# Kernel optimization log

Hardware: AMD Instinct MI355X
Metric: run time of the kernel (lower is better)

Reference implementation:

```python
import jax, jax.numpy as jnp
import numpy as np

INF = 1e8
STRIDES = (8, 16, 32, 64, 128)
SIZES_OF_INTEREST = ((0.0, 80.0), (64.0, 160.0), (128.0, 320.0), (256.0, 640.0), (512.0, 1e7))
LEVEL_HW = ((128, 128), (64, 64), (32, 32), (16, 16), (8, 8))
B, N_BOX = 4, 64
MIN_RADIUS2 = 16.0          # min_radius ** 2
DELTA = (1 - 0.8) / (1 + 0.8)
ALPHA, BETA, GAMMA = 0.25, 4.0, 2.0
SIGMOID_CLAMP = 1e-4
IGNORE_HIGH_FP = 0.85
POS_W = NEG_W = 0.5
REG_WEIGHT = 1.0


def _static():
    grids, strides, ranges, loc = [], [], [], []
    for (h, w), s, (lo, hi) in zip(LEVEL_HW, STRIDES, SIZES_OF_INTEREST):
        ys, xs = np.meshgrid(np.arange(h) * s, np.arange(w) * s, indexing='ij')
        g = np.stack([xs.reshape(-1), ys.reshape(-1)], 1).astype(np.float32) + s // 2
        grids.append(g)
        strides.append(np.full(h * w, s, np.float32))
        ranges.append(np.broadcast_to(np.array([lo, hi], np.float32), (h * w, 2)).copy())
        loc.append(h * w)
    loc = np.array(loc)
    bases = np.concatenate([[0], np.cumsum(loc * B)])[:-1]
    return np.concatenate(grids), np.concatenate(strides), np.concatenate(ranges), loc, bases

_G, _S, _R, LOC_PER_LEVEL, LEVEL_BASES = _static()
GRIDS = jnp.asarray(_G)          # [M_img, 2]
STRIDE_VEC = jnp.asarray(_S)     # [M_img]
SIZE_RANGES = jnp.asarray(_R)    # [M_img, 2]
M_IMG = GRIDS.shape[0]
M_TOT = B * M_IMG


def _assign_one(boxes):
    """GT assignment for one image. boxes [N,4] -> (reg_targets [M,4], agn_hm [M])."""
    l = GRIDS[:, 0:1] - boxes[None, :, 0]
    t = GRIDS[:, 1:2] - boxes[None, :, 1]
    r = boxes[None, :, 2] - GRIDS[:, 0:1]
    b = boxes[None, :, 3] - GRIDS[:, 1:2]
    reg = jnp.stack([l, t, r, b], 2)                              # [M,N,4]
    centers = (boxes[:, :2] + boxes[:, 2:]) / 2                   # [N,2]
    s = STRIDE_VEC[:, None, None]                                 # [M,1,1]
    cdis = (centers[None] / s).astype(jnp.int32).astype(jnp.float32) * s + s / 2  # [M,N,2]
    diff = GRIDS[:, None, :] - cdis                               # [M,N,2]
    is_peak = (diff ** 2).sum(-1) == 0
    is_in = reg.min(2) > 0
    c3x3 = (jnp.abs(diff[..., 0]) <= s[..., 0]) & (jnp.abs(diff[..., 1]) <= s[..., 0]) & is_in
    crit = jnp.sqrt(((reg[:, :, :2] + reg[:, :, 2:]) ** 2).sum(2)) / 2
    cared = (crit >= SIZE_RANGES[:, 0:1]) & (crit <= SIZE_RANGES[:, 1:2])
    reg_mask = c3x3 & cared
    dist2 = ((GRIDS[:, None, :] - centers[None]) ** 2).sum(-1)
    dist2 = jnp.where(is_peak, 0.0, dist2)
    area = (boxes[:, 2] - boxes[:, 0]) * (boxes[:, 3] - boxes[:, 1])
    radius2 = jnp.maximum(DELTA ** 2 * 2 * area, MIN_RADIUS2)
    wdist2 = dist2 / radius2[None]                                # [M,N]
    d = jnp.where(reg_mask, wdist2, INF)
    min_d = d.min(1)
    min_i = d.argmin(1)
    rt = jnp.take_along_axis(reg, min_i[:, None, None], 1)[:, 0, :]
    rt = jnp.where((min_d >= INF)[:, None], -INF, rt)
    hm = jnp.exp(-wdist2.min(1))
    hm = jnp.where(hm < 1e-4, 0.0, hm)
    return rt / STRIDE_VEC[:, None], hm


def _to_level_major(x):
    """[B, M_img, ...] -> [B*M_img, ...] in level-major (level, image, loc) order == _transpose."""
    outs, start = [], 0
    for m in LOC_PER_LEVEL:
        outs.append(x[:, start:start + int(m)].reshape((B * int(m),) + x.shape[2:]))
        start += int(m)
    return jnp.concatenate(outs, 0)


def _pos_inds(boxes):
    """_get_label_inds: flat positive indices [B*N*L] plus validity mask."""
    centers = (boxes[..., :2] + boxes[..., 2:]) / 2               # [B,N,2]
    st = jnp.asarray(STRIDES, jnp.float32)
    ci = (centers[:, :, None, :] / st[None, None, :, None]).astype(jnp.int32)  # [B,N,L,2]
    Ws = jnp.asarray([w for (_, w) in LEVEL_HW])
    loc = jnp.asarray(LOC_PER_LEVEL)
    bases = jnp.asarray(LEVEL_BASES)
    im = jnp.arange(B)[:, None, None]
    pos = bases[None, None, :] + im * loc[None, None, :] + ci[..., 1] * Ws[None, None, :] + ci[..., 0]
    crit = jnp.sqrt(((boxes[..., 2:] - boxes[..., :2]) ** 2).sum(-1)) / 2     # [B,N]
    lo = jnp.asarray([r[0] for r in SIZES_OF_INTEREST])
    hi = jnp.asarray([r[1] for r in SIZES_OF_INTEREST])
    mask = (crit[..., None] >= lo) & (crit[..., None] <= hi)
    return pos.reshape(-1), mask.reshape(-1)


def _giou_loss(pred, target):
    pl, pt, pr, pb = pred[:, 0], pred[:, 1], pred[:, 2], pred[:, 3]
    tl, tt, tr, tb = target[:, 0], target[:, 1], target[:, 2], target[:, 3]
    target_area = (tl + tr) * (tt + tb)
    pred_area = (pl + pr) * (pt + pb)
    w_i = jnp.minimum(pl, tl) + jnp.minimum(pr, tr)
    g_w = jnp.maximum(pl, tl) + jnp.maximum(pr, tr)
    h_i = jnp.minimum(pb, tb) + jnp.minimum(pt, tt)
    g_h = jnp.maximum(pb, tb) + jnp.maximum(pt, tt)
    ac = g_w * g_h + 1e-7
    inter = w_i * h_i
    union = target_area + pred_area - inter
    ious = (inter + 1.0) / (union + 1.0)
    gious = ious - (ac - union) / ac
    return 1.0 - gious


def _losses(boxes, agn_hm_pred, reg_pred):
    reg_targets, hms = jax.vmap(_assign_one)(boxes)               # [B,M,4], [B,M]
    reg_targets = _to_level_major(reg_targets)                    # [M_tot,4]
    hm = _to_level_major(hms)                                     # [M_tot]
    pos_inds, pos_mask = _pos_inds(boxes)
    num_pos_avg = jnp.maximum(pos_mask.sum().astype(jnp.float32), 1.0)

    reg_valid = reg_targets.max(1) >= 0
    safe_t = jnp.where(reg_valid[:, None], reg_targets, 1.0)
    reg_norm = jnp.maximum(reg_valid.sum().astype(jnp.float32), 1.0)
    reg_loss = REG_WEIGHT * jnp.sum(jnp.where(reg_valid, _giou_loss(reg_pred, safe_t), 0.0)) / reg_norm

    # binary heatmap focal loss (class-agnostic)
    pred = jnp.clip(jax.nn.sigmoid(agn_hm_pred), SIGMOID_CLAMP, 1.0 - SIGMOID_CLAMP)
    neg_w = jnp.power(1.0 - hm, BETA)
    idx = jnp.clip(pos_inds, 0, M_TOT - 1)
    pos_pred = pred[idx]
    pos_terms = jnp.where(pos_mask, jnp.log(pos_pred) * jnp.power(1.0 - pos_pred, GAMMA), 0.0)
    neg_terms = jnp.log(1.0 - pred) * jnp.power(pred, GAMMA) * neg_w
    neg_terms = jnp.where(pred < IGNORE_HIGH_FP, neg_terms, 0.0)
    agn_pos = POS_W * (ALPHA * (-pos_terms.sum())) / num_pos_avg
    agn_neg = NEG_W * ((1.0 - ALPHA) * (-neg_terms.sum())) / num_pos_avg
    return jnp.stack([reg_loss, agn_pos, agn_neg])


def setup_inputs() -> dict:
    key = jax.random.key(0)
    k1, k2, k3, k4, k5 = jax.random.split(key, 5)
    cxy = jax.random.uniform(k1, (B, N_BOX, 2), minval=40.0, maxval=984.0)
    wh = jax.random.uniform(k2, (B, N_BOX, 2), minval=16.0, maxval=512.0)
    boxes = jnp.concatenate([jnp.clip(cxy - wh / 2, 0.0, 1024.0),
                             jnp.clip(cxy + wh / 2, 0.0, 1024.0)], -1)
    gt_classes = jax.random.randint(k3, (B, N_BOX), 0, 4)
    agn_hm_pred = jax.random.normal(k4, (M_TOT,), jnp.float32) * 2.0 - 3.0
    reg_pred = jax.random.uniform(k5, (M_TOT, 4), jnp.float32) * 6.0 + 0.1
    return {"boxes": boxes, "gt_classes": gt_classes,
            "agn_hm_pred": agn_hm_pred, "reg_pred": reg_pred}


def reference(boxes, gt_classes, agn_hm_pred, reg_pred):
    # gt_classes unused: only_proposal=True -> class-agnostic heatmap path
    return _losses(boxes, agn_hm_pred, reg_pred)
```

## Files before the change

### kernel.cpp

```cpp
#include <hip/hip_runtime.h>
#include <math.h>

#define M_TOT 87296
#define NBLK  341
#define INF_F 100000000.0f


__global__ __launch_bounds__(256, 2) void main_kernel(
    const float* __restrict__ boxes,
    const float* __restrict__ agn,
    const float* __restrict__ reg_pred,
    float* __restrict__ partial)
{
    __shared__ float4 sBox[256];
    __shared__ float  sRed[16];

    const int t   = threadIdx.x;
    const int blk = blockIdx.x;

    if (blk == NBLK) {
        const int   BAS[5] = {0, 65536, 81920, 86016, 87040};
        const int   LOC[5] = {16384, 4096, 1024, 256, 64};
        const int   WW[5]  = {128, 64, 32, 16, 8};
        const float ST[5]  = {8.f, 16.f, 32.f, 64.f, 128.f};
        const float PLO[5] = {0.f, 64.f, 128.f, 256.f, 512.f};
        const float PHI[5] = {80.f, 160.f, 320.f, 640.f, 10000000.f};
        float psum = 0.f, pcnt = 0.f;
        for (int j = t; j < 1280; j += 256) {
            const int lev = j % 5;
            const int bn  = j / 5;
            const int b   = bn >> 6;
            const float4 bx = ((const float4*)boxes)[bn];
            const float cx = (bx.x + bx.z) * 0.5f;
            const float cy = (bx.y + bx.w) * 0.5f;
            const int cix = (int)(cx / ST[lev]);
            const int ciy = (int)(cy / ST[lev]);
            int pos = BAS[lev] + b * LOC[lev] + ciy * WW[lev] + cix;
            pos = min(max(pos, 0), M_TOT - 1);
            const float dx = bx.z - bx.x, dy = bx.w - bx.y;
            const float crit = sqrtf(dx * dx + dy * dy) * 0.5f;
            const bool msk = (crit >= PLO[lev]) && (crit <= PHI[lev]);
            const float z = agn[pos];
            float pp = 1.0f / (1.0f + expf(-z));
            pp = fminf(fmaxf(pp, 1e-4f), 1.0f - 1e-4f);
            if (msk) {
                const float om = 1.0f - pp;
                psum += logf(pp) * (om * om);
                pcnt += 1.0f;
            }
        }
        for (int off = 32; off; off >>= 1) {
            psum += __shfl_down(psum, off);
            pcnt += __shfl_down(pcnt, off);
        }
        if ((t & 63) == 0) { sRed[t >> 6] = psum; sRed[4 + (t >> 6)] = pcnt; }
        __syncthreads();
        if (t == 0) {
            partial[3 * NBLK]     = sRed[0] + sRed[1] + sRed[2] + sRed[3];
            partial[3 * NBLK + 1] = sRed[4] + sRed[5] + sRed[6] + sRed[7];
        }
        return;
    }

    const int mbase = blk << 8;
    int lev;
    if      (mbase < 65536) lev = 0;
    else if (mbase < 81920) lev = 1;
    else if (mbase < 86016) lev = 2;
    else if (mbase < 87040) lev = 3;
    else                    lev = 4;

    const int   LB_[5]   = {0, 65536, 81920, 86016, 87040};
    const int   locSh[5] = {14, 12, 10, 8, 6};
    const int   wSh[5]   = {7, 6, 5, 4, 3};
    const float SV[5]    = {8.f, 16.f, 32.f, 64.f, 128.f};
    const float LOv[5]   = {0.f, 64.f, 128.f, 256.f, 512.f};
    const float HIv[5]   = {80.f, 160.f, 320.f, 640.f, 10000000.f};

    const int   LB    = LB_[lev];
    const int   lsh   = locSh[lev];
    const int   wsh   = wSh[lev];
    const float s     = SV[lev];
    const float inv_s = 1.0f / s;
    const float half  = 0.5f * s;
    const float lo    = LOv[lev], hi = HIv[lev];

    sBox[t] = ((const float4*)boxes)[t];
    __syncthreads();

    const int g       = t >> 3;
    const int su      = t & 7;
    const int locBase = mbase + g * 8;
    const int imgBase = ((locBase - LB) >> lsh) << 6;

    const double DELTA = (1.0 - 0.8) / (1.0 + 0.8);
    const float  RADC  = (float)(DELTA * DELTA * 2.0);

    float bx1[8], by1[8], bx2[8], by2[8], bcx[8], bcy[8], bqx[8], bqy[8], bir[8];
    #pragma unroll
    for (int k = 0; k < 8; ++k) {
        const float4 A = sBox[imgBase + su + 8 * k];
        bx1[k] = A.x; by1[k] = A.y; bx2[k] = A.z; by2[k] = A.w;
        bcx[k] = (A.x + A.z) * 0.5f;
        bcy[k] = (A.y + A.w) * 0.5f;
        bqx[k] = truncf(bcx[k] * inv_s) * s + half;
        bqy[k] = truncf(bcy[k] * inv_s) * s + half;
        const float area = (A.z - A.x) * (A.w - A.y);
        bir[k] = 1.0f / fmaxf(RADC * area, 16.0f);
    }

    float minW[8], bestD[8];
    int   bestN[8];
    #pragma unroll
    for (int j = 0; j < 8; ++j) { minW[j] = INF_F; bestD[j] = INF_F; bestN[j] = 0; }

    #pragma unroll
    for (int j = 0; j < 8; ++j) {
        const int   p  = (locBase + j - LB) & ((1 << lsh) - 1);
        const float gx = (float)(p & ((1 << wsh) - 1)) * s + half;
        const float gy = (float)(p >> wsh) * s + half;
        #pragma unroll
        for (int k = 0; k < 8; ++k) {
            const float l  = gx - bx1[k];
            const float tt = gy - by1[k];
            const float rr = bx2[k] - gx;
            const float bb = by2[k] - gy;
            const bool is_in = fminf(fminf(l, tt), fminf(rr, bb)) > 0.0f;
            const float dx = gx - bqx[k], dy = gy - bqy[k];
            const bool is_peak = (dx * dx + dy * dy) == 0.0f;
            const bool c3 = (fabsf(dx) <= s) && (fabsf(dy) <= s) && is_in;
            const float wsum = l + rr, hsum = tt + bb;
            const float crit = sqrtf(wsum * wsum + hsum * hsum) * 0.5f;
            const bool msk = c3 && (crit >= lo) && (crit <= hi);
            const float ddx = gx - bcx[k], ddy = gy - bcy[k];
            const float dist2 = is_peak ? 0.0f : (ddx * ddx + ddy * ddy);
            const float w2 = dist2 * bir[k];
            minW[j] = fminf(minW[j], w2);
            const float d = msk ? w2 : INF_F;
            if (d < bestD[j]) { bestD[j] = d; bestN[j] = su + 8 * k; }
        }
    }

    unsigned long long myKey = 0; float myMinW = 0.f;
    #pragma unroll
    for (int j = 0; j < 8; ++j) {
        unsigned long long kj =
            ((unsigned long long)__float_as_uint(bestD[j]) << 6) | (unsigned)bestN[j];
        float wj = minW[j];
        #pragma unroll
        for (int m = 1; m < 8; m <<= 1) {
            const unsigned long long o = __shfl_xor(kj, m);
            kj = o < kj ? o : kj;
            wj = fminf(wj, __shfl_xor(wj, m));
        }
        if (su == j) { myKey = kj; myMinW = wj; }
    }

    const int myloc = mbase + t;
    float hmv = expf(-myMinW);
    if (hmv < 1e-4f) hmv = 0.0f;
    const float u = 1.0f - hmv;
    const float neg_w = (u * u) * (u * u);
    const float z = agn[myloc];
    float pr = 1.0f / (1.0f + expf(-z));
    pr = fminf(fmaxf(pr, 1e-4f), 1.0f - 1e-4f);
    float neg_term = 0.f, reg_term = 0.f, reg_val = 0.f;
    if (pr < 0.85f) neg_term = logf(1.0f - pr) * (pr * pr) * neg_w;

    if ((unsigned)(myKey >> 6) < __float_as_uint(INF_F)) {
        reg_val = 1.0f;
        const int n = (int)(myKey & 63);
        const int myImgBase = ((myloc - LB) >> lsh) << 6;
        const float4 A = sBox[myImgBase + n];
        const int   p  = (myloc - LB) & ((1 << lsh) - 1);
        const float gx = (float)(p & ((1 << wsh) - 1)) * s + half;
        const float gy = (float)(p >> wsh) * s + half;
        const float tl  = (gx - A.x) * inv_s;
        const float tt2 = (gy - A.y) * inv_s;
        const float tr  = (A.z - gx) * inv_s;
        const float tb  = (A.w - gy) * inv_s;
        const float4 pv = ((const float4*)reg_pred)[myloc];
        const float pl = pv.x, pt = pv.y, prr = pv.z, pb = pv.w;
        const float target_area = (tl + tr) * (tt2 + tb);
        const float pred_area   = (pl + prr) * (pt + pb);
        const float w_i = fminf(pl, tl) + fminf(prr, tr);
        const float g_w = fmaxf(pl, tl) + fmaxf(prr, tr);
        const float h_i = fminf(pb, tb) + fminf(pt, tt2);
        const float g_h = fmaxf(pb, tb) + fmaxf(pt, tt2);
        const float ac    = g_w * g_h + 1e-7f;
        const float inter = w_i * h_i;
        const float uni   = target_area + pred_area - inter;
        const float ious  = (inter + 1.0f) / (uni + 1.0f);
        const float gious = ious - (ac - uni) / ac;
        reg_term = 1.0f - gious;
    }

    float r0 = reg_term, r1 = reg_val, r2 = neg_term;
    for (int off = 32; off; off >>= 1) {
        r0 += __shfl_down(r0, off);
        r1 += __shfl_down(r1, off);
        r2 += __shfl_down(r2, off);
    }
    if ((t & 63) == 0) {
        const int w = t >> 6;
        sRed[w * 3 + 0] = r0; sRed[w * 3 + 1] = r1; sRed[w * 3 + 2] = r2;
    }
    __syncthreads();
    if (t == 0) {
        partial[blk]            = sRed[0] + sRed[3] + sRed[6] + sRed[9];
        partial[NBLK + blk]     = sRed[1] + sRed[4] + sRed[7] + sRed[10];
        partial[2 * NBLK + blk] = sRed[2] + sRed[5] + sRed[8] + sRed[11];
    }
}

__global__ __launch_bounds__(256) void finalize(
    const float* __restrict__ partial,
    float* __restrict__ out)
{
    const int t = threadIdx.x;
    float racc = 0.f, cacc = 0.f, nacc = 0.f;
    for (int j = t; j < NBLK; j += 256) {
        racc += partial[j];
        cacc += partial[NBLK + j];
        nacc += partial[2 * NBLK + j];
    }
    for (int off = 32; off; off >>= 1) {
        racc += __shfl_down(racc, off);
        cacc += __shfl_down(cacc, off);
        nacc += __shfl_down(nacc, off);
    }
    __shared__ float sr[4][3];
    if ((t & 63) == 0) {
        const int w = t >> 6;
        sr[w][0] = racc; sr[w][1] = cacc; sr[w][2] = nacc;
    }
    __syncthreads();
    if (t == 0) {
        const float RS = sr[0][0] + sr[1][0] + sr[2][0] + sr[3][0];
        const float RC = sr[0][1] + sr[1][1] + sr[2][1] + sr[3][1];
        const float NS = sr[0][2] + sr[1][2] + sr[2][2] + sr[3][2];
        const float PS = partial[3 * NBLK];
        const float PC = partial[3 * NBLK + 1];
        const float num_pos  = fmaxf(PC, 1.0f);
        const float reg_norm = fmaxf(RC, 1.0f);
        out[0] = RS / reg_norm;
        out[1] = 0.5f * (0.25f * -PS) / num_pos;
        out[2] = 0.5f * (0.75f * -NS) / num_pos;
    }
}

extern "C" void kernel_launch(void* const* d_in, const int* in_sizes, int n_in,
                              void* d_out, int out_size, void* d_ws, size_t ws_size,
                              hipStream_t stream) {
    const float* boxes    = (const float*)d_in[0];
    const float* agn      = (const float*)d_in[2];
    const float* reg_pred = (const float*)d_in[3];
    float* out = (float*)d_out;
    float* ws  = (float*)d_ws;

    main_kernel<<<NBLK + 1, 256, 0, stream>>>(boxes, agn, reg_pred, ws);
    finalize<<<1, 256, 0, stream>>>(ws, out);
}
```

Baseline: 77.64 us.

## Fuse finalize via last-block atomic, halve locations per block, precompute size mask

The finalize kernel is folded into the main kernel: a global atomic counter picks the last block to finish, and that block reduces the partials, with a memset resetting the counter before launch. Each block now covers 128 locations instead of 256, so the grid doubles and each thread handles 4 locations instead of 8. The per-box size-range test is hoisted into a bitmask because crit only depends on box width and height. In exchange, only half the threads in each block do the final loss math, and a memset plus an atomic are added per launch.

```diff
diff --git a/kernel.cpp b/kernel.cpp
--- a/kernel.cpp
+++ b/kernel.cpp
@@ -2,29 +2,34 @@
 #include <math.h>
 
 #define M_TOT 87296
-#define NBLK  341
+#define NMAIN 682
 #define INF_F 100000000.0f
 
 
-__global__ __launch_bounds__(256, 2) void main_kernel(
+__global__ __launch_bounds__(256, 2) void fused_kernel(
     const float* __restrict__ boxes,
     const float* __restrict__ agn,
     const float* __restrict__ reg_pred,
-    float* __restrict__ partial)
+    float* __restrict__ ws,
+    float* __restrict__ out)
 {
     __shared__ float4 sBox[256];
     __shared__ float  sRed[16];
+    __shared__ int    sLast;
 
     const int t   = threadIdx.x;
     const int blk = blockIdx.x;
 
-    if (blk == NBLK) {
-        const int   BAS[5] = {0, 65536, 81920, 86016, 87040};
+    const int   LB_[5]   = {0, 65536, 81920, 86016, 87040};
+    const int   locSh[5] = {14, 12, 10, 8, 6};
+    const int   wSh[5]   = {7, 6, 5, 4, 3};
+    const float SV[5]    = {8.f, 16.f, 32.f, 64.f, 128.f};
+    const float LOv[5]   = {0.f, 64.f, 128.f, 256.f, 512.f};
+    const float HIv[5]   = {80.f, 160.f, 320.f, 640.f, 10000000.f};
+
+    if (blk == NMAIN) {
         const int   LOC[5] = {16384, 4096, 1024, 256, 64};
         const int   WW[5]  = {128, 64, 32, 16, 8};
-        const float ST[5]  = {8.f, 16.f, 32.f, 64.f, 128.f};
-        const float PLO[5] = {0.f, 64.f, 128.f, 256.f, 512.f};
-        const float PHI[5] = {80.f, 160.f, 320.f, 640.f, 10000000.f};
         float psum = 0.f, pcnt = 0.f;
         for (int j = t; j < 1280; j += 256) {
             const int lev = j % 5;
@@ -33,13 +38,13 @@
             const float4 bx = ((const float4*)boxes)[bn];
             const float cx = (bx.x + bx.z) * 0.5f;
             const float cy = (bx.y + bx.w) * 0.5f;
-            const int cix = (int)(cx / ST[lev]);
-            const int ciy = (int)(cy / ST[lev]);
-            int pos = BAS[lev] + b * LOC[lev] + ciy * WW[lev] + cix;
+            const int cix = (int)(cx / SV[lev]);
+            const int ciy = (int)(cy / SV[lev]);
+            int pos = LB_[lev] + b * LOC[lev] + ciy * WW[lev] + cix;
             pos = min(max(pos, 0), M_TOT - 1);
             const float dx = bx.z - bx.x, dy = bx.w - bx.y;
             const float crit = sqrtf(dx * dx + dy * dy) * 0.5f;
-            const bool msk = (crit >= PLO[lev]) && (crit <= PHI[lev]);
+            const bool msk = (crit >= LOv[lev]) && (crit <= HIv[lev]);
             const float z = agn[pos];
             float pp = 1.0f / (1.0f + expf(-z));
             pp = fminf(fmaxf(pp, 1e-4f), 1.0f - 1e-4f);
@@ -56,173 +61,172 @@
         if ((t & 63) == 0) { sRed[t >> 6] = psum; sRed[4 + (t >> 6)] = pcnt; }
         __syncthreads();
         if (t == 0) {
-            partial[3 * NBLK]     = sRed[0] + sRed[1] + sRed[2] + sRed[3];
-            partial[3 * NBLK + 1] = sRed[4] + sRed[5] + sRed[6] + sRed[7];
-        }
-        return;
-    }
-
-    const int mbase = blk << 8;
-    int lev;
-    if      (mbase < 65536) lev = 0;
-    else if (mbase < 81920) lev = 1;
-    else if (mbase < 86016) lev = 2;
-    else if (mbase < 87040) lev = 3;
-    else                    lev = 4;
-
-    const int   LB_[5]   = {0, 65536, 81920, 86016, 87040};
-    const int   locSh[5] = {14, 12, 10, 8, 6};
-    const int   wSh[5]   = {7, 6, 5, 4, 3};
-    const float SV[5]    = {8.f, 16.f, 32.f, 64.f, 128.f};
-    const float LOv[5]   = {0.f, 64.f, 128.f, 256.f, 512.f};
-    const float HIv[5]   = {80.f, 160.f, 320.f, 640.f, 10000000.f};
-
-    const int   LB    = LB_[lev];
-    const int   lsh   = locSh[lev];
-    const int   wsh   = wSh[lev];
-    const float s     = SV[lev];
-    const float inv_s = 1.0f / s;
-    const float half  = 0.5f * s;
-    const float lo    = LOv[lev], hi = HIv[lev];
-
-    sBox[t] = ((const float4*)boxes)[t];
-    __syncthreads();
-
-    const int g       = t >> 3;
-    const int su      = t & 7;
-    const int locBase = mbase + g * 8;
-    const int imgBase = ((locBase - LB) >> lsh) << 6;
-
-    const double DELTA = (1.0 - 0.8) / (1.0 + 0.8);
-    const float  RADC  = (float)(DELTA * DELTA * 2.0);
-
-    float bx1[8], by1[8], bx2[8], by2[8], bcx[8], bcy[8], bqx[8], bqy[8], bir[8];
-    #pragma unroll
-    for (int k = 0; k < 8; ++k) {
-        const float4 A = sBox[imgBase + su + 8 * k];
-        bx1[k] = A.x; by1[k] = A.y; bx2[k] = A.z; by2[k] = A.w;
-        bcx[k] = (A.x + A.z) * 0.5f;
-        bcy[k] = (A.y + A.w) * 0.5f;
-        bqx[k] = truncf(bcx[k] * inv_s) * s + half;
-        bqy[k] = truncf(bcy[k] * inv_s) * s + half;
-        const float area = (A.z - A.x) * (A.w - A.y);
-        bir[k] = 1.0f / fmaxf(RADC * area, 16.0f);
-    }
-
-    float minW[8], bestD[8];
-    int   bestN[8];
-    #pragma unroll
-    for (int j = 0; j < 8; ++j) { minW[j] = INF_F; bestD[j] = INF_F; bestN[j] = 0; }
-
-    #pragma unroll
-    for (int j = 0; j < 8; ++j) {
-        const int   p  = (locBase + j - LB) & ((1 << lsh) - 1);
-        const float gx = (float)(p & ((1 << wsh) - 1)) * s + half;
-        const float gy = (float)(p >> wsh) * s + half;
+            ws[4 + 3 * NMAIN]     = sRed[0] + sRed[1] + sRed[2] + sRed[3];
+            ws[4 + 3 * NMAIN + 1] = sRed[4] + sRed[5] + sRed[6] + sRed[7];
+        }
+    } else {
+        const int mbase = blk << 7;
+        int lev;
+        if      (mbase < 65536) lev = 0;
+        else if (mbase < 81920) lev = 1;
+        else if (mbase < 86016) lev = 2;
+        else if (mbase < 87040) lev = 3;
+        else                    lev = 4;
+
+        const int   LB    = LB_[lev];
+        const int   lsh   = locSh[lev];
+        const int   wsh   = wSh[lev];
+        const float s     = SV[lev];
+        const float inv_s = 1.0f / s;
+        const float half  = 0.5f * s;
+        const float lo    = LOv[lev], hi = HIv[lev];
+
+        sBox[t] = ((const float4*)boxes)[t];
+        __syncthreads();
+
+        const int g       = t >> 3;
+        const int su      = t & 7;
+        const int locBase = mbase + g * 4;
+        const int imgBase = ((locBase - LB) >> lsh) << 6;
+
+        const double DELTA = (1.0 - 0.8) / (1.0 + 0.8);
+        const float  RADC  = (float)(DELTA * DELTA * 2.0);
+
+        float bx1[8], by1[8], bx2[8], by2[8], bcx[8], bcy[8], bqx[8], bqy[8], bir[8];
+        int caredMask = 0;
         #pragma unroll
         for (int k = 0; k < 8; ++k) {
-            const float l  = gx - bx1[k];
-            const float tt = gy - by1[k];
-            const float rr = bx2[k] - gx;
-            const float bb = by2[k] - gy;
-            const bool is_in = fminf(fminf(l, tt), fminf(rr, bb)) > 0.0f;
-            const float dx = gx - bqx[k], dy = gy - bqy[k];
-            const bool is_peak = (dx * dx + dy * dy) == 0.0f;
-            const bool c3 = (fabsf(dx) <= s) && (fabsf(dy) <= s) && is_in;
-            const float wsum = l + rr, hsum = tt + bb;
-            const float crit = sqrtf(wsum * wsum + hsum * hsum) * 0.5f;
-            const bool msk = c3 && (crit >= lo) && (crit <= hi);
-            const float ddx = gx - bcx[k], ddy = gy - bcy[k];
-            const float dist2 = is_peak ? 0.0f : (ddx * ddx + ddy * ddy);
-            const float w2 = dist2 * bir[k];
-            minW[j] = fminf(minW[j], w2);
-            const float d = msk ? w2 : INF_F;
-            if (d < bestD[j]) { bestD[j] = d; bestN[j] = su + 8 * k; }
-        }
-    }
-
-    unsigned long long myKey = 0; float myMinW = 0.f;
-    #pragma unroll
-    for (int j = 0; j < 8; ++j) {
-        unsigned long long kj =
-            ((unsigned long long)__float_as_uint(bestD[j]) << 6) | (unsigned)bestN[j];
-        float wj = minW[j];
-        #pragma unroll
-        for (int m = 1; m < 8; m <<= 1) {
-            const unsigned long long o = __shfl_xor(kj, m);
-            kj = o < kj ? o : kj;
-            wj = fminf(wj, __shfl_xor(wj, m));
-        }
-        if (su == j) { myKey = kj; myMinW = wj; }
-    }
-
-    const int myloc = mbase + t;
-    float hmv = expf(-myMinW);
-    if (hmv < 1e-4f) hmv = 0.0f;
-    const float u = 1.0f - hmv;
-    const float neg_w = (u * u) * (u * u);
-    const float z = agn[myloc];
-    float pr = 1.0f / (1.0f + expf(-z));
-    pr = fminf(fmaxf(pr, 1e-4f), 1.0f - 1e-4f);
-    float neg_term = 0.f, reg_term = 0.f, reg_val = 0.f;
-    if (pr < 0.85f) neg_term = logf(1.0f - pr) * (pr * pr) * neg_w;
-
-    if ((unsigned)(myKey >> 6) < __float_as_uint(INF_F)) {
-        reg_val = 1.0f;
-        const int n = (int)(myKey & 63);
-        const int myImgBase = ((myloc - LB) >> lsh) << 6;
-        const float4 A = sBox[myImgBase + n];
-        const int   p  = (myloc - LB) & ((1 << lsh) - 1);
-        const float gx = (float)(p & ((1 << wsh) - 1)) * s + half;
-        const float gy = (float)(p >> wsh) * s + half;
-        const float tl  = (gx - A.x) * inv_s;
-        const float tt2 = (gy - A.y) * inv_s;
-        const float tr  = (A.z - gx) * inv_s;
-        const float tb  = (A.w - gy) * inv_s;
-        const float4 pv = ((const float4*)reg_pred)[myloc];
-        const float pl = pv.x, pt = pv.y, prr = pv.z, pb = pv.w;
-        const float target_area = (tl + tr) * (tt2 + tb);
-        const float pred_area   = (pl + prr) * (pt + pb);
-        const float w_i = fminf(pl, tl) + fminf(prr, tr);
-        const float g_w = fmaxf(pl, tl) + fmaxf(prr, tr);
-        const float h_i = fminf(pb, tb) + fminf(pt, tt2);
-        const float g_h = fmaxf(pb, tb) + fmaxf(pt, tt2);
-        const float ac    = g_w * g_h + 1e-7f;
-        const float inter = w_i * h_i;
-        const float uni   = target_area + pred_area - inter;
-        const float ious  = (inter + 1.0f) / (uni + 1.0f);
-        const float gious = ious - (ac - uni) / ac;
-        reg_term = 1.0f - gious;
-    }
-
-    float r0 = reg_term, r1 = reg_val, r2 = neg_term;
-    for (int off = 32; off; off >>= 1) {
-        r0 += __shfl_down(r0, off);
-        r1 += __shfl_down(r1, off);
-        r2 += __shfl_down(r2, off);
-    }
-    if ((t & 63) == 0) {
-        const int w = t >> 6;
-        sRed[w * 3 + 0] = r0; sRed[w * 3 + 1] = r1; sRed[w * 3 + 2] = r2;
-    }
+            const float4 A = sBox[imgBase + su + 8 * k];
+            bx1[k] = A.x; by1[k] = A.y; bx2[k] = A.z; by2[k] = A.w;
+            bcx[k] = (A.x + A.z) * 0.5f;
+            bcy[k] = (A.y + A.w) * 0.5f;
+            bqx[k] = truncf(bcx[k] * inv_s) * s + half;
+            bqy[k] = truncf(bcy[k] * inv_s) * s + half;
+            const float area = (A.z - A.x) * (A.w - A.y);
+            bir[k] = 1.0f / fmaxf(RADC * area, 16.0f);
+            const float bw = A.z - A.x, bh = A.w - A.y;
+            const float crit = sqrtf(bw * bw + bh * bh) * 0.5f;
+            caredMask |= ((crit >= lo) && (crit <= hi)) ? (1 << k) : 0;
+        }
+
+        float minW[4], bestD[4];
+        int   bestN[4];
+        #pragma unroll
+        for (int j = 0; j < 4; ++j) { minW[j] = INF_F; bestD[j] = INF_F; bestN[j] = 0; }
+
+        #pragma unroll
+        for (int j = 0; j < 4; ++j) {
+            const int   p  = (locBase + j - LB) & ((1 << lsh) - 1);
+            const float gx = (float)(p & ((1 << wsh) - 1)) * s + half;
+            const float gy = (float)(p >> wsh) * s + half;
+            #pragma unroll
+            for (int k = 0; k < 8; ++k) {
+                const float l  = gx - bx1[k];
+                const float tt = gy - by1[k];
+                const float rr = bx2[k] - gx;
+                const float bb = by2[k] - gy;
+                const bool is_in = fminf(fminf(l, tt), fminf(rr, bb)) > 0.0f;
+                const float dx = gx - bqx[k], dy = gy - bqy[k];
+                const bool is_peak = (dx * dx + dy * dy) == 0.0f;
+                const bool msk = (fabsf(dx) <= s) && (fabsf(dy) <= s) && is_in
+                                 && ((caredMask >> k) & 1);
+                const float ddx = gx - bcx[k], ddy = gy - bcy[k];
+                const float dist2 = is_peak ? 0.0f : (ddx * ddx + ddy * ddy);
+                const float w2 = dist2 * bir[k];
+                minW[j] = fminf(minW[j], w2);
+                const float d = msk ? w2 : INF_F;
+                if (d < bestD[j]) { bestD[j] = d; bestN[j] = su + 8 * k; }
+            }
+        }
+
+        unsigned long long myKey = ~0ULL; float myMinW = INF_F;
+        #pragma unroll
+        for (int j = 0; j < 4; ++j) {
+            unsigned long long kj =
+                ((unsigned long long)__float_as_uint(bestD[j]) << 6) | (unsigned)bestN[j];
+            float wj = minW[j];
+            #pragma unroll
+            for (int m = 1; m < 8; m <<= 1) {
+                const unsigned long long o = __shfl_xor(kj, m);
+                kj = o < kj ? o : kj;
+                wj = fminf(wj, __shfl_xor(wj, m));
+            }
+            if (su == j) { myKey = kj; myMinW = wj; }
+        }
+
+        float neg_term = 0.f, reg_term = 0.f, reg_val = 0.f;
+        if (su < 4) {
+            const int myloc = locBase + su;
+            float hmv = expf(-myMinW);
+            if (hmv < 1e-4f) hmv = 0.0f;
+            const float u = 1.0f - hmv;
+            const float neg_w = (u * u) * (u * u);
+            const float z = agn[myloc];
+            float pr = 1.0f / (1.0f + expf(-z));
+            pr = fminf(fmaxf(pr, 1e-4f), 1.0f - 1e-4f);
+            if (pr < 0.85f) neg_term = logf(1.0f - pr) * (pr * pr) * neg_w;
+
+            if ((unsigned)(myKey >> 6) < __float_as_uint(INF_F)) {
+                reg_val = 1.0f;
+                const int n = (int)(myKey & 63);
+                const float4 A = sBox[imgBase + n];
+                const int   p  = (myloc - LB) & ((1 << lsh) - 1);
+                const float gx = (float)(p & ((1 << wsh) - 1)) * s + half;
+                const float gy = (float)(p >> wsh) * s + half;
+                const float tl  = (gx - A.x) * inv_s;
+                const float tt2 = (gy - A.y) * inv_s;
+                const float tr  = (A.z - gx) * inv_s;
+                const float tb  = (A.w - gy) * inv_s;
+                const float4 pv = ((const float4*)reg_pred)[myloc];
+                const float pl = pv.x, pt = pv.y, prr = pv.z, pb = pv.w;
+                const float target_area = (tl + tr) * (tt2 + tb);
+                const float pred_area   = (pl + prr) * (pt + pb);
+                const float w_i = fminf(pl, tl) + fminf(prr, tr);
+                const float g_w = fmaxf(pl, tl) + fmaxf(prr, tr);
+                const float h_i = fminf(pb, tb) + fminf(pt, tt2);
+                const float g_h = fmaxf(pb, tb) + fmaxf(pt, tt2);
+                const float ac    = g_w * g_h + 1e-7f;
+                const float inter = w_i * h_i;
+                const float uni   = target_area + pred_area - inter;
+                const float ious  = (inter + 1.0f) / (uni + 1.0f);
+                const float gious = ious - (ac - uni) / ac;
+                reg_term = 1.0f - gious;
+            }
+        }
+
+        float r0 = reg_term, r1 = reg_val, r2 = neg_term;
+        for (int off = 32; off; off >>= 1) {
+            r0 += __shfl_down(r0, off);
+            r1 += __shfl_down(r1, off);
+            r2 += __shfl_down(r2, off);
+        }
+        if ((t & 63) == 0) {
+            const int w = t >> 6;
+            sRed[w * 3 + 0] = r0; sRed[w * 3 + 1] = r1; sRed[w * 3 + 2] = r2;
+        }
+        __syncthreads();
+        if (t == 0) {
+            ws[4 + blk]             = sRed[0] + sRed[3] + sRed[6] + sRed[9];
+            ws[4 + NMAIN + blk]     = sRed[1] + sRed[4] + sRed[7] + sRed[10];
+            ws[4 + 2 * NMAIN + blk] = sRed[2] + sRed[5] + sRed[8] + sRed[11];
+        }
+    }
+
     __syncthreads();
     if (t == 0) {
-        partial[blk]            = sRed[0] + sRed[3] + sRed[6] + sRed[9];
-        partial[NBLK + blk]     = sRed[1] + sRed[4] + sRed[7] + sRed[10];
-        partial[2 * NBLK + blk] = sRed[2] + sRed[5] + sRed[8] + sRed[11];
-    }
-}
-
-__global__ __launch_bounds__(256) void finalize(
-    const float* __restrict__ partial,
-    float* __restrict__ out)
-{
-    const int t = threadIdx.x;
+        __threadfence();
+        const int old = atomicAdd((int*)ws, 1);
+        sLast = (old == NMAIN);
+    }
+    __syncthreads();
+    if (!sLast) return;
+    __threadfence();
+
     float racc = 0.f, cacc = 0.f, nacc = 0.f;
-    for (int j = t; j < NBLK; j += 256) {
-        racc += partial[j];
-        cacc += partial[NBLK + j];
-        nacc += partial[2 * NBLK + j];
+    for (int j = t; j < NMAIN; j += 256) {
+        racc += ws[4 + j];
+        cacc += ws[4 + NMAIN + j];
+        nacc += ws[4 + 2 * NMAIN + j];
     }
     for (int off = 32; off; off >>= 1) {
         racc += __shfl_down(racc, off);
@@ -239,8 +243,8 @@
         const float RS = sr[0][0] + sr[1][0] + sr[2][0] + sr[3][0];
         const float RC = sr[0][1] + sr[1][1] + sr[2][1] + sr[3][1];
         const float NS = sr[0][2] + sr[1][2] + sr[2][2] + sr[3][2];
-        const float PS = partial[3 * NBLK];
-        const float PC = partial[3 * NBLK + 1];
+        const float PS = ws[4 + 3 * NMAIN];
+        const float PC = ws[4 + 3 * NMAIN + 1];
         const float num_pos  = fmaxf(PC, 1.0f);
         const float reg_norm = fmaxf(RC, 1.0f);
         out[0] = RS / reg_norm;
@@ -258,6 +262,6 @@
     float* out = (float*)d_out;
     float* ws  = (float*)d_ws;
 
-    main_kernel<<<NBLK + 1, 256, 0, stream>>>(boxes, agn, reg_pred, ws);
-    finalize<<<1, 256, 0, stream>>>(ws, out);
+    hipMemsetAsync(d_ws, 0, 4, stream);
+    fused_kernel<<<NMAIN + 1, 256, 0, stream>>>(boxes, agn, reg_pred, ws, out);
 }
```

After: 81.40 us. 4.8% more time.
